# Performance work log

Measured on AMD Instinct MI355X. Metric: run time of the kernel, lower is better.

Reference implementation:

```python
import jax, jax.numpy as jnp
import numpy as np
from functools import partial

N_OSC = 50
N_PER = 40
DT = 0.001
STEPS = 700
HALF_PI = float(np.pi / 2)
# limb constants (simple antagonist-muscle one-link limb, as in TorchOneLinkMuscleLimb)
R_MOM = 0.02      # muscle moment arm
L0 = 0.1          # muscle length at angle 0
INERTIA = 1e-3
DAMP = 0.01
K_MUS = 50.0
L_REST = 0.05
TAU_M = 0.05


def get_m1_length(theta):
    return L0 - R_MOM * theta


def get_m2_length(theta):
    return L0 + R_MOM * theta


def limb_f(l_state, activation):
    # l_state: (B,4) = (angle, ang. velocity, m1 length, m2 length); activation: (B,2)
    theta, omega, l1, l2 = l_state[:, 0], l_state[:, 1], l_state[:, 2], l_state[:, 3]
    f1 = jax.nn.relu(activation[:, 0]) * K_MUS * jax.nn.relu(l1 - L_REST)
    f2 = jax.nn.relu(activation[:, 1]) * K_MUS * jax.nn.relu(l2 - L_REST)
    domega = (R_MOM * (f2 - f1) - DAMP * omega) / INERTIA
    dl1 = (get_m1_length(theta) - l1) / TAU_M
    dl2 = (get_m2_length(theta) - l2) / TAU_M
    return jnp.stack([omega, domega, dl1, dl2], axis=1)


def setup_inputs() -> dict:
    key = jax.random.key(0)
    ks = jax.random.split(key, 16)
    B = 4096
    x = jax.random.normal(ks[0], (B, 2), dtype=jnp.float32) * 0.5
    def lin(k, out_d, in_d, scale=None):
        s = (1.0 / np.sqrt(in_d)) if scale is None else scale
        kw, kb = jax.random.split(k)
        w = jax.random.uniform(kw, (out_d, in_d), jnp.float32, -s, s)
        b = jax.random.uniform(kb, (out_d,), jnp.float32, -s, s)
        return w, b
    fc1_w, fc1_b = lin(ks[1], 128, 2)
    fc2_w, fc2_b = lin(ks[2], 128, 128)
    fc3_w, fc3_b = lin(ks[3], N_OSC * 2, 128)
    fcd_w, fcd_b = lin(ks[4], 2, 128)
    fcd_w = fcd_w / 100.0
    fcd_b = fcd_b * 0.0 + 0.1
    fc4_w, fc4_b = lin(ks[5], 32, N_OSC * N_PER)
    fc5_w, fc5_b = lin(ks[6], 2, 32)
    fc5_w = fc5_w / 10000.0
    fc5_b = fc5_b * 0.0
    # NEF oscillator populations: encoders (unit vectors), biases, decoders
    enc = jax.random.normal(ks[7], (N_OSC, N_PER, 2), dtype=jnp.float32)
    enc = enc / jnp.linalg.norm(enc, axis=-1, keepdims=True)
    osc_bias = jax.random.uniform(ks[8], (N_OSC, N_PER), jnp.float32, -1.0, 1.0)
    dec = jax.random.normal(ks[9], (N_OSC, 2, N_PER), dtype=jnp.float32) * 0.05
    return dict(x=x, fc1_w=fc1_w, fc1_b=fc1_b, fc2_w=fc2_w, fc2_b=fc2_b,
                fc3_w=fc3_w, fc3_b=fc3_b, fcd_w=fcd_w, fcd_b=fcd_b,
                enc=enc, osc_bias=osc_bias, dec=dec,
                fc4_w=fc4_w, fc4_b=fc4_b, fc5_w=fc5_w, fc5_b=fc5_b)


def _forward(x, fc1_w, fc1_b, fc2_w, fc2_b, fc3_w, fc3_b, fcd_w, fcd_b,
             enc, osc_bias, dec, fc4_w, fc4_b, fc5_w, fc5_b):
    B = x.shape[0]
    current_angle = x[:, 0]
    h = jax.nn.relu(x @ fc1_w.T + fc1_b)
    direct = h @ fcd_w.T + fcd_b                     # (B, 2)
    h2 = jax.nn.relu(h @ fc2_w.T + fc2_b)
    xo = h2 @ fc3_w.T + fc3_b                        # (B, 2*N_OSC)
    o0 = jnp.transpose(xo.reshape(B, N_OSC, 2), (1, 0, 2))   # (O, B, 2)
    l0 = jnp.stack([current_angle, jnp.zeros_like(current_angle),
                    get_m1_length(current_angle), get_m2_length(current_angle)], axis=1)

    def step(carry, _):
        o_states, l_state = carry
        # NEF activities: relu(encoders . state + bias) per oscillator
        a = jax.nn.relu(jnp.einsum('opd,obd->obp', enc, o_states) + osc_bias[:, None, :])  # (O,B,P)
        deriv = jnp.einsum('odp,obp->obd', dec, a)
        o_states = o_states + DT * deriv
        activities = jnp.transpose(a, (1, 0, 2)).reshape(B, N_OSC * N_PER)  # (B, 2000)
        b1 = jax.nn.relu(activities @ fc4_w.T + fc4_b)
        activation = b1 @ fc5_w.T + fc5_b + direct    # (B, 2)
        l_new = l_state + DT * limb_f(l_state, activation)
        pos, vel = l_new[:, 0], l_new[:, 1]
        in_bounds = (pos > -HALF_PI) & (pos < HALF_PI)
        l_new = jnp.stack([jnp.clip(pos, -HALF_PI, HALF_PI),
                           jnp.where(in_bounds, vel, 0.0),
                           l_new[:, 2], l_new[:, 3]], axis=1)
        return (o_states, l_new), (l_new, activation)

    (_, _), (l_states, activations) = jax.lax.scan(step, (o0, l0), None, length=STEPS)
    return l_states, activations


@jax.jit
def reference(x, fc1_w, fc1_b, fc2_w, fc2_b, fc3_w, fc3_b, fcd_w, fcd_b,
              enc, osc_bias, dec, fc4_w, fc4_b, fc5_w, fc5_b):
    return _forward(x, fc1_w, fc1_b, fc2_w, fc2_b, fc3_w, fc3_b, fcd_w, fcd_b,
                    enc, osc_bias, dec, fc4_w, fc4_b, fc5_w, fc5_b)
```

## Files before the change

### kernel.cpp

```cpp
#include <hip/hip_runtime.h>

#define NTHR 1024
#define NB   16
#define NOSC 50
#define NPER 40
#define KTOT 2000
#define KPAD 2048
#define NSTEP 700
#define BATCH 4096
#define B1STR 36
#define OS_STR 36
#define HALF_PI 1.57079632679489662f
#define ACT_OFF ((size_t)NSTEP * BATCH * 4)

typedef _Float16 v8h __attribute__((ext_vector_type(8)));
typedef _Float16 h2_t __attribute__((ext_vector_type(2)));
typedef float v4f __attribute__((ext_vector_type(4)));

__device__ _Float16 g_w4[32 * KPAD];

__device__ __forceinline__ float fdot2f(float a_bits, float b_bits, float acc) {
    h2_t a = __builtin_bit_cast(h2_t, a_bits);
    h2_t b = __builtin_bit_cast(h2_t, b_bits);
#if __has_builtin(__builtin_amdgcn_fdot2)
    return __builtin_amdgcn_fdot2(a, b, acc, false);
#else
    return fmaf((float)a[0], (float)b[0], fmaf((float)a[1], (float)b[1], acc));
#endif
}

__device__ __forceinline__ float dot4(float4 a, float4 b, float acc) {
    acc = fmaf(a.x, b.x, acc);
    acc = fmaf(a.y, b.y, acc);
    acc = fmaf(a.z, b.z, acc);
    acc = fmaf(a.w, b.w, acc);
    return acc;
}

__device__ __forceinline__ float pkrtz(float a, float b) {
    auto q = __builtin_amdgcn_cvt_pkrtz(a, b);
    return __builtin_bit_cast(float, q);
}

__device__ __forceinline__ float cvt2rtn(float a, float b) {
    h2_t u; u[0] = (_Float16)a; u[1] = (_Float16)b;
    return __builtin_bit_cast(float, u);
}

__global__ void prep_f16(const float* __restrict__ fc4_w) {
    int tid = blockIdx.x * blockDim.x + threadIdx.x;
    int j = tid >> 11, k = tid & 2047;
    g_w4[j * KPAD + k] = (k < KTOT) ? (_Float16)fc4_w[j * KTOT + k] : (_Float16)0.f;
}

__global__ __launch_bounds__(NTHR)
void net_main(const float* __restrict__ x,
              const float* __restrict__ fc1_w, const float* __restrict__ fc1_b,
              const float* __restrict__ fc2_w, const float* __restrict__ fc2_b,
              const float* __restrict__ fc3_w, const float* __restrict__ fc3_b,
              const float* __restrict__ fcd_w, const float* __restrict__ fcd_b,
              const float* __restrict__ enc,   const float* __restrict__ osc_bias,
              const float* __restrict__ dec,
              const float* __restrict__ fc4_b,
              const float* __restrict__ fc5_w, const float* __restrict__ fc5_b,
              float* __restrict__ out)
{
    __shared__ __align__(16) _Float16 act_sh[256 * 128];
    __shared__ __align__(16) float part[16 * 2 * 256];
    __shared__ __align__(16) float os_sh[NOSC * OS_STR];
    __shared__ __align__(16) float b1s[NB * B1STR];
    __shared__ __align__(16) float dir[NB * 2];

    const int t    = threadIdx.x;
    const int lane = t & 63;
    const int wv   = t >> 6;
    const int b0   = blockIdx.x * NB;

    float* h  = (float*)act_sh;
    float* h2 = (float*)act_sh + NB * 128;

    #pragma unroll
    for (int ii = 0; ii < 2; ++ii) {
        int task = t + ii * NTHR;
        int b = task >> 7, i = task & 127;
        float x0 = x[(b0 + b) * 2 + 0];
        float x1 = x[(b0 + b) * 2 + 1];
        float v = fmaf(x0, fc1_w[2 * i], fmaf(x1, fc1_w[2 * i + 1], fc1_b[i]));
        h[b * 128 + i] = fmaxf(v, 0.f);
    }
    __syncthreads();
    #pragma unroll
    for (int ii = 0; ii < 2; ++ii) {
        int task = t + ii * NTHR;
        int b = task >> 7, i = task & 127;
        float acc = fc2_b[i];
        #pragma unroll 4
        for (int k = 0; k < 128; k += 4)
            acc = dot4(*(const float4*)&fc2_w[i * 128 + k],
                       *(const float4*)&h[b * 128 + k], acc);
        h2[b * 128 + i] = fmaxf(acc, 0.f);
    }
    if (t < NB * 2) {
        int b = t >> 1, j = t & 1;
        float acc = fcd_b[j];
        #pragma unroll 4
        for (int k = 0; k < 128; k += 4)
            acc = dot4(*(const float4*)&fcd_w[j * 128 + k],
                       *(const float4*)&h[b * 128 + k], acc);
        dir[b * 2 + j] = acc;
    }
    __syncthreads();
    #pragma unroll
    for (int ii = 0; ii < 2; ++ii) {
        int task = t + ii * NTHR;
        if (task < NOSC * NB * 2) {
            int o = task >> 5, r = task & 31, b = r >> 1;
            int row = o * 2 + (r & 1);
            float acc = fc3_b[row];
            #pragma unroll 4
            for (int k = 0; k < 128; k += 4)
                acc = dot4(*(const float4*)&fc3_w[row * 128 + k],
                           *(const float4*)&h2[b * 128 + k], acc);
            os_sh[o * OS_STR + r] = acc;
        }
    }
    const int my_oct = t >> 2;
    float4 e0 = {0,0,0,0}, e1 = {0,0,0,0}, e2 = {0,0,0,0}, e3 = {0,0,0,0};
    float4 bi0 = {0,0,0,0}, bi1 = {0,0,0,0};
    int my_o = 0;
    if (my_oct < 250) {
        const float4* ep = (const float4*)&enc[my_oct * 16];
        e0 = ep[0]; e1 = ep[1]; e2 = ep[2]; e3 = ep[3];
        const float4* bp = (const float4*)&osc_bias[my_oct * 8];
        bi0 = bp[0]; bi1 = bp[1];
        my_o = my_oct / 5;
    }
    float4 dd0[5], dd1[5];
    if (t < NOSC * NB) {
        int o = t >> 4;
        const float* d0p = &dec[(o * 2 + 0) * 40];
        const float* d1p = &dec[(o * 2 + 1) * 40];
        #pragma unroll
        for (int c = 0; c < 5; ++c) {
            dd0[c].x = cvt2rtn(d0p[c*8+0], d0p[c*8+1]);
            dd0[c].y = cvt2rtn(d0p[c*8+2], d0p[c*8+3]);
            dd0[c].z = cvt2rtn(d0p[c*8+4], d0p[c*8+5]);
            dd0[c].w = cvt2rtn(d0p[c*8+6], d0p[c*8+7]);
            dd1[c].x = cvt2rtn(d1p[c*8+0], d1p[c*8+1]);
            dd1[c].y = cvt2rtn(d1p[c*8+2], d1p[c*8+3]);
            dd1[c].z = cvt2rtn(d1p[c*8+4], d1p[c*8+5]);
            dd1[c].w = cvt2rtn(d1p[c*8+6], d1p[c*8+7]);
        }
    }
    float theta = 0.f, omega = 0.f, l1 = 0.f, l2 = 0.f, bs0 = 0.f, bs1 = 0.f;
    const int cb = t - 960;
    if (cb >= 0 && cb < NB) {
        theta = x[(b0 + cb) * 2 + 0];
        l1 = fmaf(-0.02f, theta, 0.1f);
        l2 = fmaf( 0.02f, theta, 0.1f);
    }
    __syncthreads();
    if (cb >= 0 && cb < NB) {
        bs0 = dir[cb * 2 + 0] + fc5_b[0];
        bs1 = dir[cb * 2 + 1] + fc5_b[1];
    }
    if (t < 768) act_sh[32000 + t] = (_Float16)0.f;

    const int n_col = lane & 15, quad = lane >> 4;
    const int lidx  = lane ^ (quad << 2);
    int a_off[4];
    #pragma unroll
    for (int ks4 = 0; ks4 < 4; ++ks4) {
        int oct = (wv * 4 + ks4) * 4 + quad;
        a_off[ks4] = oct * 128 + ((n_col ^ (oct & 15)) * 8);
    }
    v8h wr[8];
    {
        const _Float16* wp = &g_w4[n_col * KPAD + wv * 128 + quad * 8];
        #pragma unroll
        for (int ks4 = 0; ks4 < 4; ++ks4) {
            wr[ks4]     = *(const v8h*)&wp[ks4 * 32];
            wr[4 + ks4] = *(const v8h*)&wp[16 * KPAD + ks4 * 32];
        }
    }

    auto phaseA = [&]() {
        if (my_oct < 250) {
            const int i4 = (t & 3) << 2;
            float4 osA = *(const float4*)&os_sh[my_o * OS_STR + i4 * 2];
            float4 osB = *(const float4*)&os_sh[my_o * OS_STR + i4 * 2 + 4];
            #pragma unroll
            for (int ii = 0; ii < 4; ++ii) {
                int b = i4 + ii;
                float osx = (ii == 0) ? osA.x : (ii == 1) ? osA.z : (ii == 2) ? osB.x : osB.z;
                float osy = (ii == 0) ? osA.y : (ii == 1) ? osA.w : (ii == 2) ? osB.y : osB.w;
                float r0 = fmaxf(fmaf(e0.x, osx, fmaf(e0.y, osy, bi0.x)), 0.f);
                float r1 = fmaxf(fmaf(e0.z, osx, fmaf(e0.w, osy, bi0.y)), 0.f);
                float r2 = fmaxf(fmaf(e1.x, osx, fmaf(e1.y, osy, bi0.z)), 0.f);
                float r3 = fmaxf(fmaf(e1.z, osx, fmaf(e1.w, osy, bi0.w)), 0.f);
                float r4 = fmaxf(fmaf(e2.x, osx, fmaf(e2.y, osy, bi1.x)), 0.f);
                float r5 = fmaxf(fmaf(e2.z, osx, fmaf(e2.w, osy, bi1.y)), 0.f);
                float r6 = fmaxf(fmaf(e3.x, osx, fmaf(e3.y, osy, bi1.z)), 0.f);
                float r7 = fmaxf(fmaf(e3.z, osx, fmaf(e3.w, osy, bi1.w)), 0.f);
                float4 pk;
                pk.x = pkrtz(r0, r1);
                pk.y = pkrtz(r2, r3);
                pk.z = pkrtz(r4, r5);
                pk.w = pkrtz(r6, r7);
                *(float4*)&act_sh[my_oct * 128 + ((b ^ my_oct) & 15) * 8] = pk;
            }
        }
    };

    phaseA();
    __syncthreads();

    for (int s = 0; s < NSTEP; ++s) {
        {
            v4f c0 = {0.f, 0.f, 0.f, 0.f}, c1 = {0.f, 0.f, 0.f, 0.f};
            #pragma unroll
            for (int ks4 = 0; ks4 < 4; ++ks4) {
                v8h a = *(const v8h*)&act_sh[a_off[ks4]];
                c0 = __builtin_amdgcn_mfma_f32_16x16x32_f16(a, wr[ks4],     c0, 0, 0, 0);
                c1 = __builtin_amdgcn_mfma_f32_16x16x32_f16(a, wr[4 + ks4], c1, 0, 0, 0);
            }
            *(v4f*)&part[(wv * 2 + 0) * 256 + lidx * 4] = c0;
            *(v4f*)&part[(wv * 2 + 1) * 256 + lidx * 4] = c1;
        }
        if (t < NOSC * NB) {
            int o = t >> 4, b = t & 15;
            float p0 = 0.f, p1 = 0.f, q0 = 0.f, q1 = 0.f;
            #pragma unroll
            for (int c = 0; c < 5; ++c) {
                int oct = o * 5 + c;
                float4 af = *(const float4*)&act_sh[oct * 128 + ((b ^ oct) & 15) * 8];
                p0 = fdot2f(af.x, dd0[c].x, p0); p1 = fdot2f(af.y, dd0[c].y, p1);
                p0 = fdot2f(af.z, dd0[c].z, p0); p1 = fdot2f(af.w, dd0[c].w, p1);
                q0 = fdot2f(af.x, dd1[c].x, q0); q1 = fdot2f(af.y, dd1[c].y, q1);
                q0 = fdot2f(af.z, dd1[c].z, q0); q1 = fdot2f(af.w, dd1[c].w, q1);
            }
            float2 osv = *(const float2*)&os_sh[o * OS_STR + b * 2];
            osv.x += 0.001f * (p0 + p1);
            osv.y += 0.001f * (q0 + q1);
            *(float2*)&os_sh[o * OS_STR + b * 2] = osv;
        } else if (cb >= 0 && cb < NB && s > 0) {
            float a0 = bs0, a1 = bs1;
            #pragma unroll
            for (int i = 0; i < 32; i += 4) {
                float4 bv = *(const float4*)&b1s[cb * B1STR + i];
                a0 = dot4(bv, *(const float4*)&fc5_w[i],      a0);
                a1 = dot4(bv, *(const float4*)&fc5_w[32 + i], a1);
            }
            float f1v = fmaxf(a0, 0.f) * 50.f * fmaxf(l1 - 0.05f, 0.f);
            float f2v = fmaxf(a1, 0.f) * 50.f * fmaxf(l2 - 0.05f, 0.f);
            float domega = (0.02f * (f2v - f1v) - 0.01f * omega) / 0.001f;
            float dl1 = ((0.1f - 0.02f * theta) - l1) / 0.05f;
            float dl2 = ((0.1f + 0.02f * theta) - l2) / 0.05f;
            float pos = fmaf(0.001f, omega,  theta);
            float vel = fmaf(0.001f, domega, omega);
            l1 = fmaf(0.001f, dl1, l1);
            l2 = fmaf(0.001f, dl2, l2);
            bool inb = (pos > -HALF_PI) && (pos < HALF_PI);
            float posc = fminf(fmaxf(pos, -HALF_PI), HALF_PI);
            vel = inb ? vel : 0.f;
            theta = posc;
            omega = vel;
            float4 lo; lo.x = posc; lo.y = vel; lo.z = l1; lo.w = l2;
            *(float4*)&out[((size_t)(s - 1) * BATCH + (b0 + cb)) * 4] = lo;
            float2 ao; ao.x = a0; ao.y = a1;
            *(float2*)&out[ACT_OFF + ((size_t)(s - 1) * BATCH + (b0 + cb)) * 2] = ao;
        }
        __syncthreads();

        if (t < 512) {
            int b = t & 15, j = t >> 4;
            int g = j >> 4, n = j & 15;
            int Lp = (b >> 2) * 16 + (n ^ ((b >> 2) << 2));
            int base = g * 256 + Lp * 4 + (b & 3);
            float sum = 0.f;
            #pragma unroll
            for (int w = 0; w < 16; ++w)
                sum += part[w * 512 + base];
            b1s[b * B1STR + j] = fmaxf(sum + fc4_b[j], 0.f);
        }
        phaseA();
        __syncthreads();
    }

    if (cb >= 0 && cb < NB) {
        const int s = NSTEP - 1;
        float a0 = bs0, a1 = bs1;
        #pragma unroll
        for (int i = 0; i < 32; i += 4) {
            float4 bv = *(const float4*)&b1s[cb * B1STR + i];
            a0 = dot4(bv, *(const float4*)&fc5_w[i],      a0);
            a1 = dot4(bv, *(const float4*)&fc5_w[32 + i], a1);
        }
        float f1v = fmaxf(a0, 0.f) * 50.f * fmaxf(l1 - 0.05f, 0.f);
        float f2v = fmaxf(a1, 0.f) * 50.f * fmaxf(l2 - 0.05f, 0.f);
        float domega = (0.02f * (f2v - f1v) - 0.01f * omega) / 0.001f;
        float dl1 = ((0.1f - 0.02f * theta) - l1) / 0.05f;
        float dl2 = ((0.1f + 0.02f * theta) - l2) / 0.05f;
        float pos = fmaf(0.001f, omega,  theta);
        float vel = fmaf(0.001f, domega, omega);
        l1 = fmaf(0.001f, dl1, l1);
        l2 = fmaf(0.001f, dl2, l2);
        bool inb = (pos > -HALF_PI) && (pos < HALF_PI);
        float posc = fminf(fmaxf(pos, -HALF_PI), HALF_PI);
        vel = inb ? vel : 0.f;
        float4 lo; lo.x = posc; lo.y = vel; lo.z = l1; lo.w = l2;
        *(float4*)&out[((size_t)s * BATCH + (b0 + cb)) * 4] = lo;
        float2 ao; ao.x = a0; ao.y = a1;
        *(float2*)&out[ACT_OFF + ((size_t)s * BATCH + (b0 + cb)) * 2] = ao;
    }
}

extern "C" void kernel_launch(void* const* d_in, const int* in_sizes, int n_in,
                              void* d_out, int out_size, void* d_ws, size_t ws_size,
                              hipStream_t stream) {
    (void)in_sizes; (void)n_in; (void)d_ws; (void)ws_size; (void)out_size;
    const float* x_     = (const float*)d_in[0];
    const float* fc1_w  = (const float*)d_in[1];
    const float* fc1_b  = (const float*)d_in[2];
    const float* fc2_w  = (const float*)d_in[3];
    const float* fc2_b  = (const float*)d_in[4];
    const float* fc3_w  = (const float*)d_in[5];
    const float* fc3_b  = (const float*)d_in[6];
    const float* fcd_w  = (const float*)d_in[7];
    const float* fcd_b  = (const float*)d_in[8];
    const float* enc    = (const float*)d_in[9];
    const float* oscb   = (const float*)d_in[10];
    const float* dec    = (const float*)d_in[11];
    const float* fc4_w  = (const float*)d_in[12];
    const float* fc4_b  = (const float*)d_in[13];
    const float* fc5_w  = (const float*)d_in[14];
    const float* fc5_b  = (const float*)d_in[15];
    float* out = (float*)d_out;

    hipLaunchKernelGGL(prep_f16, dim3(256), dim3(256), 0, stream, fc4_w);
    hipLaunchKernelGGL(net_main, dim3(BATCH / NB), dim3(NTHR), 0, stream,
                       x_, fc1_w, fc1_b, fc2_w, fc2_b, fc3_w, fc3_b,
                       fcd_w, fcd_b, enc, oscb, dec, fc4_b,
                       fc5_w, fc5_b, out);
}
```

Measured before the change: 2.005 ms.

## Split waves into dedicated MFMA and oscillator-derivative roles per step

The fc4 MFMA reduction now runs on the first 8 waves only, each covering twice the K range with doubled weight registers, so the cross-wave partial-sum buffer and its reduction are halved. The other 8 waves handle the oscillator derivative update concurrently, with some threads doing two batch columns. The limb-update thread also moves into that wave group. The aim is to overlap the MFMA work with the derivative dot products instead of serialising them within the same waves, at the cost of more registers per thread and uneven per-wave load.

```diff
diff --git a/kernel.cpp b/kernel.cpp
--- a/kernel.cpp
+++ b/kernel.cpp
@@ -66,7 +66,7 @@
               float* __restrict__ out)
 {
     __shared__ __align__(16) _Float16 act_sh[256 * 128];
-    __shared__ __align__(16) float part[16 * 2 * 256];
+    __shared__ __align__(16) float part[8 * 2 * 256];
     __shared__ __align__(16) float os_sh[NOSC * OS_STR];
     __shared__ __align__(16) float b1s[NB * B1STR];
     __shared__ __align__(16) float dir[NB * 2];
@@ -135,11 +135,15 @@
         bi0 = bp[0]; bi1 = bp[1];
         my_o = my_oct / 5;
     }
+    const int di = t - 512;
+    int d_o = 0, d_b = 0;
+    bool dual = false;
     float4 dd0[5], dd1[5];
-    if (t < NOSC * NB) {
-        int o = t >> 4;
-        const float* d0p = &dec[(o * 2 + 0) * 40];
-        const float* d1p = &dec[(o * 2 + 1) * 40];
+    if (di >= 0) {
+        if (di < 288) { dual = true; d_o = di >> 3; d_b = (di & 7) * 2; }
+        else          { int task = di + 288; d_o = task >> 4; d_b = task & 15; }
+        const float* d0p = &dec[(d_o * 2 + 0) * 40];
+        const float* d1p = &dec[(d_o * 2 + 1) * 40];
         #pragma unroll
         for (int c = 0; c < 5; ++c) {
             dd0[c].x = cvt2rtn(d0p[c*8+0], d0p[c*8+1]);
@@ -153,7 +157,7 @@
         }
     }
     float theta = 0.f, omega = 0.f, l1 = 0.f, l2 = 0.f, bs0 = 0.f, bs1 = 0.f;
-    const int cb = t - 960;
+    const int cb = t - 1008;
     if (cb >= 0 && cb < NB) {
         theta = x[(b0 + cb) * 2 + 0];
         l1 = fmaf(-0.02f, theta, 0.1f);
@@ -168,19 +172,19 @@
 
     const int n_col = lane & 15, quad = lane >> 4;
     const int lidx  = lane ^ (quad << 2);
-    int a_off[4];
+    int a_off[8];
     #pragma unroll
-    for (int ks4 = 0; ks4 < 4; ++ks4) {
-        int oct = (wv * 4 + ks4) * 4 + quad;
-        a_off[ks4] = oct * 128 + ((n_col ^ (oct & 15)) * 8);
-    }
-    v8h wr[8];
-    {
-        const _Float16* wp = &g_w4[n_col * KPAD + wv * 128 + quad * 8];
+    for (int ks = 0; ks < 8; ++ks) {
+        int oct = wv * 32 + ks * 4 + quad;
+        a_off[ks] = (oct & 255) * 128 + ((n_col ^ (oct & 15)) * 8);
+    }
+    v8h wr[16];
+    if (t < 512) {
+        const _Float16* wp = &g_w4[n_col * KPAD + wv * 256 + quad * 8];
         #pragma unroll
-        for (int ks4 = 0; ks4 < 4; ++ks4) {
-            wr[ks4]     = *(const v8h*)&wp[ks4 * 32];
-            wr[4 + ks4] = *(const v8h*)&wp[16 * KPAD + ks4 * 32];
+        for (int ks = 0; ks < 8; ++ks) {
+            wr[ks]     = *(const v8h*)&wp[ks * 32];
+            wr[8 + ks] = *(const v8h*)&wp[16 * KPAD + ks * 32];
         }
     }
 
@@ -212,63 +216,81 @@
         }
     };
 
+    auto derivDot = [&](int b, float& pOut, float& qOut) {
+        float p0 = 0.f, p1 = 0.f, q0 = 0.f, q1 = 0.f;
+        #pragma unroll
+        for (int c = 0; c < 5; ++c) {
+            int oct = d_o * 5 + c;
+            float4 af = *(const float4*)&act_sh[oct * 128 + ((b ^ oct) & 15) * 8];
+            p0 = fdot2f(af.x, dd0[c].x, p0); p1 = fdot2f(af.y, dd0[c].y, p1);
+            p0 = fdot2f(af.z, dd0[c].z, p0); p1 = fdot2f(af.w, dd0[c].w, p1);
+            q0 = fdot2f(af.x, dd1[c].x, q0); q1 = fdot2f(af.y, dd1[c].y, q1);
+            q0 = fdot2f(af.z, dd1[c].z, q0); q1 = fdot2f(af.w, dd1[c].w, q1);
+        }
+        pOut = p0 + p1;
+        qOut = q0 + q1;
+    };
+
     phaseA();
     __syncthreads();
 
     for (int s = 0; s < NSTEP; ++s) {
-        {
+        if (t < 512) {
             v4f c0 = {0.f, 0.f, 0.f, 0.f}, c1 = {0.f, 0.f, 0.f, 0.f};
             #pragma unroll
-            for (int ks4 = 0; ks4 < 4; ++ks4) {
-                v8h a = *(const v8h*)&act_sh[a_off[ks4]];
-                c0 = __builtin_amdgcn_mfma_f32_16x16x32_f16(a, wr[ks4],     c0, 0, 0, 0);
-                c1 = __builtin_amdgcn_mfma_f32_16x16x32_f16(a, wr[4 + ks4], c1, 0, 0, 0);
+            for (int ks = 0; ks < 8; ++ks) {
+                v8h a = *(const v8h*)&act_sh[a_off[ks]];
+                c0 = __builtin_amdgcn_mfma_f32_16x16x32_f16(a, wr[ks],     c0, 0, 0, 0);
+                c1 = __builtin_amdgcn_mfma_f32_16x16x32_f16(a, wr[8 + ks], c1, 0, 0, 0);
             }
             *(v4f*)&part[(wv * 2 + 0) * 256 + lidx * 4] = c0;
             *(v4f*)&part[(wv * 2 + 1) * 256 + lidx * 4] = c1;
-        }
-        if (t < NOSC * NB) {
-            int o = t >> 4, b = t & 15;
-            float p0 = 0.f, p1 = 0.f, q0 = 0.f, q1 = 0.f;
-            #pragma unroll
-            for (int c = 0; c < 5; ++c) {
-                int oct = o * 5 + c;
-                float4 af = *(const float4*)&act_sh[oct * 128 + ((b ^ oct) & 15) * 8];
-                p0 = fdot2f(af.x, dd0[c].x, p0); p1 = fdot2f(af.y, dd0[c].y, p1);
-                p0 = fdot2f(af.z, dd0[c].z, p0); p1 = fdot2f(af.w, dd0[c].w, p1);
-                q0 = fdot2f(af.x, dd1[c].x, q0); q1 = fdot2f(af.y, dd1[c].y, q1);
-                q0 = fdot2f(af.z, dd1[c].z, q0); q1 = fdot2f(af.w, dd1[c].w, q1);
+        } else {
+            if (dual) {
+                float pA, qA, pB, qB;
+                derivDot(d_b,     pA, qA);
+                derivDot(d_b + 1, pB, qB);
+                float4 osv = *(const float4*)&os_sh[d_o * OS_STR + d_b * 2];
+                osv.x += 0.001f * pA;
+                osv.y += 0.001f * qA;
+                osv.z += 0.001f * pB;
+                osv.w += 0.001f * qB;
+                *(float4*)&os_sh[d_o * OS_STR + d_b * 2] = osv;
+            } else {
+                float p, q;
+                derivDot(d_b, p, q);
+                float2 osv = *(const float2*)&os_sh[d_o * OS_STR + d_b * 2];
+                osv.x += 0.001f * p;
+                osv.y += 0.001f * q;
+                *(float2*)&os_sh[d_o * OS_STR + d_b * 2] = osv;
             }
-            float2 osv = *(const float2*)&os_sh[o * OS_STR + b * 2];
-            osv.x += 0.001f * (p0 + p1);
-            osv.y += 0.001f * (q0 + q1);
-            *(float2*)&os_sh[o * OS_STR + b * 2] = osv;
-        } else if (cb >= 0 && cb < NB && s > 0) {
-            float a0 = bs0, a1 = bs1;
-            #pragma unroll
-            for (int i = 0; i < 32; i += 4) {
-                float4 bv = *(const float4*)&b1s[cb * B1STR + i];
-                a0 = dot4(bv, *(const float4*)&fc5_w[i],      a0);
-                a1 = dot4(bv, *(const float4*)&fc5_w[32 + i], a1);
+            if (cb >= 0 && cb < NB && s > 0) {
+                float a0 = bs0, a1 = bs1;
+                #pragma unroll
+                for (int i = 0; i < 32; i += 4) {
+                    float4 bv = *(const float4*)&b1s[cb * B1STR + i];
+                    a0 = dot4(bv, *(const float4*)&fc5_w[i],      a0);
+                    a1 = dot4(bv, *(const float4*)&fc5_w[32 + i], a1);
+                }
+                float f1v = fmaxf(a0, 0.f) * 50.f * fmaxf(l1 - 0.05f, 0.f);
+                float f2v = fmaxf(a1, 0.f) * 50.f * fmaxf(l2 - 0.05f, 0.f);
+                float domega = (0.02f * (f2v - f1v) - 0.01f * omega) / 0.001f;
+                float dl1 = ((0.1f - 0.02f * theta) - l1) / 0.05f;
+                float dl2 = ((0.1f + 0.02f * theta) - l2) / 0.05f;
+                float pos = fmaf(0.001f, omega,  theta);
+                float vel = fmaf(0.001f, domega, omega);
+                l1 = fmaf(0.001f, dl1, l1);
+                l2 = fmaf(0.001f, dl2, l2);
+                bool inb = (pos > -HALF_PI) && (pos < HALF_PI);
+                float posc = fminf(fmaxf(pos, -HALF_PI), HALF_PI);
+                vel = inb ? vel : 0.f;
+                theta = posc;
+                omega = vel;
+                float4 lo; lo.x = posc; lo.y = vel; lo.z = l1; lo.w = l2;
+                *(float4*)&out[((size_t)(s - 1) * BATCH + (b0 + cb)) * 4] = lo;
+                float2 ao; ao.x = a0; ao.y = a1;
+                *(float2*)&out[ACT_OFF + ((size_t)(s - 1) * BATCH + (b0 + cb)) * 2] = ao;
             }
-            float f1v = fmaxf(a0, 0.f) * 50.f * fmaxf(l1 - 0.05f, 0.f);
-            float f2v = fmaxf(a1, 0.f) * 50.f * fmaxf(l2 - 0.05f, 0.f);
-            float domega = (0.02f * (f2v - f1v) - 0.01f * omega) / 0.001f;
-            float dl1 = ((0.1f - 0.02f * theta) - l1) / 0.05f;
-            float dl2 = ((0.1f + 0.02f * theta) - l2) / 0.05f;
-            float pos = fmaf(0.001f, omega,  theta);
-            float vel = fmaf(0.001f, domega, omega);
-            l1 = fmaf(0.001f, dl1, l1);
-            l2 = fmaf(0.001f, dl2, l2);
-            bool inb = (pos > -HALF_PI) && (pos < HALF_PI);
-            float posc = fminf(fmaxf(pos, -HALF_PI), HALF_PI);
-            vel = inb ? vel : 0.f;
-            theta = posc;
-            omega = vel;
-            float4 lo; lo.x = posc; lo.y = vel; lo.z = l1; lo.w = l2;
-            *(float4*)&out[((size_t)(s - 1) * BATCH + (b0 + cb)) * 4] = lo;
-            float2 ao; ao.x = a0; ao.y = a1;
-            *(float2*)&out[ACT_OFF + ((size_t)(s - 1) * BATCH + (b0 + cb)) * 2] = ao;
         }
         __syncthreads();
 
@@ -279,7 +301,7 @@
             int base = g * 256 + Lp * 4 + (b & 3);
             float sum = 0.f;
             #pragma unroll
-            for (int w = 0; w < 16; ++w)
+            for (int w = 0; w < 8; ++w)
                 sum += part[w * 512 + base];
             b1s[b * B1STR + j] = fmaxf(sum + fc4_b[j], 0.f);
         }
```

Measured after the change: 4.060 ms. 2.02x slower.
